# Optimization experiments

Measured on AMD Instinct MI355X. Metric: run time of the kernel, lower is better.

Reference implementation:

```python
import jax, jax.numpy as jnp
import numpy as np

N_EMBD = 1024
HEAD_SIZE = 64
BLOCK = 4096
B = 4

def setup_inputs() -> dict:
    key = jax.random.key(0)
    k1, k2, k3, k4, k5, k6 = jax.random.split(key, 6)
    x = jax.random.normal(k1, (B, BLOCK, N_EMBD), dtype=jnp.float32)
    freqs_cos = jax.random.uniform(k2, (BLOCK, HEAD_SIZE // 2), dtype=jnp.float32)
    freqs_sin = jax.random.uniform(k3, (BLOCK, HEAD_SIZE // 2), dtype=jnp.float32)
    # bias-free Linear weights, stored as [in, out] so y = x @ W
    s = 1.0 / np.sqrt(N_EMBD)
    Wq = jax.random.normal(k4, (N_EMBD, HEAD_SIZE), dtype=jnp.float32) * s
    Wk = jax.random.normal(k5, (N_EMBD, HEAD_SIZE), dtype=jnp.float32) * s
    Wv = jax.random.normal(k6, (N_EMBD, HEAD_SIZE), dtype=jnp.float32) * s
    return {"x": x, "Wq": Wq, "Wk": Wk, "Wv": Wv,
            "freqs_cos": freqs_cos, "freqs_sin": freqs_sin}

def _rope(t, cos, sin):
    # t: [B,T,hs]; cos/sin: [T, hs//2]. Rotate consecutive (even,odd) pairs.
    tr = t[..., 0::2]
    ti = t[..., 1::2]
    cos = cos[None, :, :]
    sin = sin[None, :, :]
    out_r = tr * cos - ti * sin
    out_i = tr * sin + ti * cos
    return jnp.stack([out_r, out_i], axis=-1).reshape(t.shape)

def reference(x, Wq, Wk, Wv, freqs_cos, freqs_sin):
    B_, T, C = x.shape
    q = x @ Wq  # [B,T,hs]
    k = x @ Wk
    v = x @ Wv
    q = _rope(q, freqs_cos[:T], freqs_sin[:T])
    k = _rope(k, freqs_cos[:T], freqs_sin[:T])
    scale = k.shape[-1] ** -0.5
    wei = jnp.einsum('bqd,bkd->bqk', q, k) * scale  # [B,T,T]
    mask = jnp.tril(jnp.ones((T, T), dtype=bool))
    wei = jnp.where(mask[None], wei, -jnp.inf)
    wei = jax.nn.softmax(wei, axis=-1)
    return jnp.einsum('bqk,bkd->bqd', wei, v)
```

## Files before the change

### kernel.cpp

```cpp
#include <hip/hip_runtime.h>
#include <hip/hip_bf16.h>
#include <stdint.h>

#define TSEQ 4096
#define CEMB 1024
#define DH   64
#define NB   4
#define NCHUNK 4

typedef __attribute__((ext_vector_type(8))) short bf16x8;
typedef __attribute__((ext_vector_type(4))) float f32x4;
typedef __attribute__((ext_vector_type(4))) float f4;
typedef unsigned short u16;

__device__ __forceinline__ u16 f2bf(float f) {
  __hip_bfloat16 h = __float2bfloat16(f);
  return *(u16*)&h;
}

__device__ __forceinline__ int swz(int row, int colbyte) {
  return row * 128 + (colbyte ^ ((row & 7) << 4));
}

__global__ void prep_w(const float* __restrict__ Wq, const float* __restrict__ Wk,
                       const float* __restrict__ Wv, u16* __restrict__ wt) {
  int idx = blockIdx.x * 256 + threadIdx.x;
  if (idx >= 3 * DH * CEMB) return;
  int m = idx >> 16;
  int r = idx & 65535;
  int k = r >> 6, n = r & 63;
  const float* W = (m == 0) ? Wq : (m == 1) ? Wk : Wv;
  wt[(size_t)m * 65536 + n * 1024 + k] = f2bf(W[r]);
}

__launch_bounds__(256)
__global__ void qkv_gemm(const float* __restrict__ x, const u16* __restrict__ wt,
                         const float* __restrict__ fc, const float* __restrict__ fs,
                         u16* __restrict__ q_ws, u16* __restrict__ k_ws,
                         u16* __restrict__ vt_ws) {
  const int tid  = threadIdx.x;
  const int lane = tid & 63;
  const int w    = tid >> 6;
  const int l15  = lane & 15;
  const int lhi  = lane >> 4;
  const int rg   = w & 1;
  const int cg   = w >> 1;
  const int m0   = blockIdx.x * 32;

  const float* xr = x + (size_t)(m0 + rg * 16 + l15) * CEMB;
  const u16*   wb = wt + (size_t)(cg * 96 + l15) * CEMB;

  const f32x4 z4 = {0.f, 0.f, 0.f, 0.f};
  f32x4 acc[6];
#pragma unroll
  for (int j = 0; j < 6; ++j) acc[j] = z4;

#pragma unroll 2
  for (int k0 = 0; k0 < CEMB; k0 += 64) {
    bf16x8 af[2];
#pragma unroll
    for (int kk = 0; kk < 2; ++kk) {
      const float* s = xr + k0 + kk * 32 + lhi * 8;
      f4 a = *(const f4*)s;
      f4 b = *(const f4*)(s + 4);
      af[kk][0] = (short)f2bf(a[0]); af[kk][1] = (short)f2bf(a[1]);
      af[kk][2] = (short)f2bf(a[2]); af[kk][3] = (short)f2bf(a[3]);
      af[kk][4] = (short)f2bf(b[0]); af[kk][5] = (short)f2bf(b[1]);
      af[kk][6] = (short)f2bf(b[2]); af[kk][7] = (short)f2bf(b[3]);
    }
#pragma unroll
    for (int kk = 0; kk < 2; ++kk)
#pragma unroll
      for (int nc = 0; nc < 6; ++nc) {
        bf16x8 bfr = *(const bf16x8*)(wb + (size_t)nc * 16 * CEMB + k0 + kk * 32 + lhi * 8);
        acc[nc] = __builtin_amdgcn_mfma_f32_16x16x32_bf16(af[kk], bfr, acc[nc], 0, 0, 0);
      }
  }

#pragma unroll
  for (int nc = 0; nc < 6; ++nc) {
    int gcol = cg * 96 + nc * 16 + l15;
    int mat  = gcol >> 6;
    int col  = gcol & 63;
#pragma unroll
    for (int r = 0; r < 4; ++r) {
      float v = acc[nc][r];
      float o = __shfl_xor(v, 1);
      int row = m0 + rg * 16 + lhi * 4 + r;
      int b = row >> 12, t = row & 4095;
      if (mat == 2) {
        vt_ws[((size_t)(b * DH + col)) * TSEQ + t] = f2bf(v);
      } else {
        int p = col >> 1;
        float cv = fc[t * 32 + p], sv = fs[t * 32 + p];
        float outv = ((col & 1) == 0) ? (v * cv - o * sv)
                                      : (o * sv + v * cv);
        if (mat == 0) outv *= 0.125f;
        u16* dst = (mat == 0) ? q_ws : k_ws;
        dst[(size_t)row * DH + col] = f2bf(outv);
      }
    }
  }
}

#define ATT_LOADKV(KV0) \
    _Pragma("unroll") for (int it = 0; it < 2; ++it) { \
      int gg = it * 256 + tid, row_ = gg >> 3, cc_ = gg & 7; \
      kreg[it] = *(const bf16x8*)(kb + (size_t)((KV0) + row_) * DH + cc_ * 8); \
      vreg[it] = *(const bf16x8*)(vb + (size_t)row_ * TSEQ + (KV0) + cc_ * 8); }
#define ATT_WRITEKV \
    _Pragma("unroll") for (int it = 0; it < 2; ++it) { \
      int gg = it * 256 + tid, row_ = gg >> 3, cc_ = gg & 7; \
      *(bf16x8*)((char*)kt + swz(row_, cc_ << 4)) = kreg[it]; \
      *(bf16x8*)((char*)vts + swz(row_, cc_ << 4)) = vreg[it]; }

__launch_bounds__(256)
__global__ void attn_partial(const u16* __restrict__ q_ws, const u16* __restrict__ k_ws,
                             const u16* __restrict__ vt_ws, float* __restrict__ po,
                             float* __restrict__ pml) {
  const int g  = blockIdx.x;
  const int j  = blockIdx.y;
  const int b  = g >> 6;
  const int r0 = g & 63;
  const int qt = (j & 1) ? (63 - r0) : r0;
  const int c  = j;

  const int ntiles = qt + 1;
  const int cnt    = (ntiles + NCHUNK - 1) / NCHUNK;
  const int t0     = c * cnt;
  if (t0 >= ntiles) return;
  const int t1     = min(t0 + cnt, ntiles);

  __shared__ __align__(16) u16 kt[64 * 64];
  __shared__ __align__(16) u16 vts[64 * 64];
  __shared__ __align__(16) u16 pt2[4 * 16 * 64];

  const int tid  = threadIdx.x;
  const int lane = tid & 63;
  const int w    = tid >> 6;
  const int l15  = lane & 15;
  const int lhi  = lane >> 4;
  const int q0   = qt * 64;

  const u16* qb = q_ws + (size_t)b * TSEQ * DH;
  const u16* kb = k_ws + (size_t)b * TSEQ * DH;
  const u16* vb = vt_ws + (size_t)b * DH * TSEQ;
  char* ptw = (char*)pt2 + w * 2048;

  bf16x8 aq[2];
  {
    int qrow = q0 + w * 16 + l15;
#pragma unroll
    for (int kk = 0; kk < 2; ++kk)
      aq[kk] = *(const bf16x8*)(qb + (size_t)qrow * DH + kk * 32 + lhi * 8);
  }

  const f32x4 z4 = {0.f, 0.f, 0.f, 0.f};
  f32x4 oacc[4] = {z4, z4, z4, z4};
  float m_r[4], l_p[4];
#pragma unroll
  for (int r = 0; r < 4; ++r) { m_r[r] = -1e30f; l_p[r] = 0.f; }

  const int myqbase = q0 + w * 16 + lhi * 4;

  bf16x8 kreg[2], vreg[2];

  for (int kv = t0; kv < t1; ++kv) {
    const int kv0 = kv * 64;
    ATT_LOADKV(kv0)
    __syncthreads();
    ATT_WRITEKV
    __syncthreads();

    f32x4 sacc[4] = {z4, z4, z4, z4};
    __builtin_amdgcn_s_setprio(1);
#pragma unroll
    for (int kk = 0; kk < 2; ++kk) {
#pragma unroll
      for (int cb = 0; cb < 4; ++cb) {
        bf16x8 bk = *(const bf16x8*)((char*)kt + swz(cb * 16 + l15, (kk * 32 + lhi * 8) * 2));
        sacc[cb] = __builtin_amdgcn_mfma_f32_16x16x32_bf16(aq[kk], bk, sacc[cb], 0, 0, 0);
      }
    }
    __builtin_amdgcn_s_setprio(0);

    if (kv0 == q0) {
#pragma unroll
      for (int cb = 0; cb < 4; ++cb)
#pragma unroll
        for (int r = 0; r < 4; ++r) {
          int ki = kv0 + cb * 16 + l15;
          int qi = myqbase + r;
          if (ki > qi) sacc[cb][r] = -1e30f;
        }
    }
    float mx[4];
#pragma unroll
    for (int r = 0; r < 4; ++r)
      mx[r] = fmaxf(fmaxf(sacc[0][r], sacc[1][r]), fmaxf(sacc[2][r], sacc[3][r]));
#pragma unroll
    for (int s = 1; s <= 8; s <<= 1)
#pragma unroll
      for (int r = 0; r < 4; ++r) mx[r] = fmaxf(mx[r], __shfl_xor(mx[r], s));
    bool skip = true;
#pragma unroll
    for (int r = 0; r < 4; ++r) skip = skip && (mx[r] <= m_r[r] + 8.f);
    if (!__all(skip)) {
#pragma unroll
      for (int r = 0; r < 4; ++r) {
        float mn = fmaxf(m_r[r], mx[r]);
        float fac = __expf(m_r[r] - mn);
        m_r[r] = mn;
        l_p[r] *= fac;
#pragma unroll
        for (int nc = 0; nc < 4; ++nc) oacc[nc][r] *= fac;
      }
    }
#pragma unroll
    for (int cb = 0; cb < 4; ++cb)
#pragma unroll
      for (int r = 0; r < 4; ++r) {
        float p = __expf(sacc[cb][r] - m_r[r]);
        l_p[r] += p;
        *(u16*)(ptw + swz(lhi * 4 + r, (cb * 16 + l15) * 2)) = f2bf(p);
      }
    bf16x8 ap[2];
#pragma unroll
    for (int kk = 0; kk < 2; ++kk)
      ap[kk] = *(const bf16x8*)(ptw + swz(l15, (kk * 32 + lhi * 8) * 2));
    __builtin_amdgcn_s_setprio(1);
#pragma unroll
    for (int kk = 0; kk < 2; ++kk)
#pragma unroll
      for (int nc = 0; nc < 4; ++nc) {
        bf16x8 bv = *(const bf16x8*)((char*)vts + swz(nc * 16 + l15, (kk * 32 + lhi * 8) * 2));
        oacc[nc] = __builtin_amdgcn_mfma_f32_16x16x32_bf16(ap[kk], bv, oacc[nc], 0, 0, 0);
      }
    __builtin_amdgcn_s_setprio(0);
  }

#pragma unroll
  for (int s = 1; s <= 8; s <<= 1)
#pragma unroll
    for (int r = 0; r < 4; ++r) l_p[r] += __shfl_xor(l_p[r], s);

  const int slot = ((b * 64 + qt) * NCHUNK + c);
  float* o_out = po + (size_t)slot * (64 * 64);
#pragma unroll
  for (int nc = 0; nc < 4; ++nc)
#pragma unroll
    for (int r = 0; r < 4; ++r) {
      int rloc = w * 16 + lhi * 4 + r;
      o_out[rloc * 64 + nc * 16 + l15] = oacc[nc][r];
    }
#pragma unroll
  for (int r = 0; r < 4; ++r) {
    if (l15 == 0) {
      int rloc = w * 16 + lhi * 4 + r;
      pml[(size_t)slot * 128 + rloc]      = m_r[r];
      pml[(size_t)slot * 128 + 64 + rloc] = l_p[r];
    }
  }
}

__launch_bounds__(256)
__global__ void attn_combine(const float* __restrict__ po, const float* __restrict__ pml,
                             float* __restrict__ out) {
  int idx = blockIdx.x * 256 + threadIdx.x;
  int d   = idx & 63;
  int t   = (idx >> 6) & 4095;
  int b   = idx >> 18;
  int qt  = t >> 6;
  int rloc = t & 63;
  int ntiles = qt + 1;
  int cnt = (ntiles + NCHUNK - 1) / NCHUNK;

  float m_c[NCHUNK], l_c[NCHUNK], o_c[NCHUNK];
  float M = -1e30f;
#pragma unroll
  for (int c = 0; c < NCHUNK; ++c) {
    bool valid = (c * cnt < ntiles);
    int slot = ((b * 64 + qt) * NCHUNK + c);
    m_c[c] = valid ? pml[(size_t)slot * 128 + rloc]      : -1e30f;
    l_c[c] = valid ? pml[(size_t)slot * 128 + 64 + rloc] : 0.f;
    o_c[c] = valid ? po[(size_t)slot * (64 * 64) + rloc * 64 + d] : 0.f;
    M = fmaxf(M, m_c[c]);
  }
  float den = 0.f, num = 0.f;
#pragma unroll
  for (int c = 0; c < NCHUNK; ++c) {
    float e = __expf(m_c[c] - M);
    den += e * l_c[c];
    num += e * o_c[c];
  }
  out[idx] = num / den;
}

extern "C" void kernel_launch(void* const* d_in, const int* in_sizes, int n_in,
                              void* d_out, int out_size, void* d_ws, size_t ws_size,
                              hipStream_t stream) {
  const float* x  = (const float*)d_in[0];
  const float* Wq = (const float*)d_in[1];
  const float* Wk = (const float*)d_in[2];
  const float* Wv = (const float*)d_in[3];
  const float* fc = (const float*)d_in[4];
  const float* fs = (const float*)d_in[5];
  float* out = (float*)d_out;

  char* ws = (char*)d_ws;
  u16*   wt    = (u16*)(ws);
  u16*   q_ws  = (u16*)(ws + (1u << 19));
  u16*   k_ws  = (u16*)(ws + (1u << 19) + (1u << 21));
  u16*   vt_ws = (u16*)(ws + (1u << 19) + (2u << 21));
  float* po    = (float*)(ws + (1u << 19) + (3u << 21));
  float* pml   = (float*)(ws + (1u << 19) + (3u << 21) + (1u << 24));

  prep_w<<<(3 * DH * CEMB + 255) / 256, 256, 0, stream>>>(Wq, Wk, Wv, wt);
  qkv_gemm<<<dim3(512), 256, 0, stream>>>(x, wt, fc, fs, q_ws, k_ws, vt_ws);
  attn_partial<<<dim3(256, NCHUNK), 256, 0, stream>>>(q_ws, k_ws, vt_ws, po, pml);
  attn_combine<<<dim3((NB * TSEQ * DH) / 256), 256, 0, stream>>>(po, pml, out);
}
```

Baseline: 192.7 us.

## Pre-swizzle weights into MFMA fragment order and double-buffer QKV GEMM loads

The weight prep kernel now writes bf16 weights already arranged in per-lane MFMA B-fragment order, so each lane reads a contiguous 16-byte chunk and a wave's load is fully coalesced. The QKV GEMM main loop is rewritten as a software-pipelined, double-buffered loop that issues the next k-step's x and weight loads before running the current step's MFMAs, to hide global-load latency. Launch bounds now request two blocks per CU. The two register buffers raise register pressure, which could limit occupancy or cause spills.

```diff
diff --git a/kernel.cpp b/kernel.cpp
--- a/kernel.cpp
+++ b/kernel.cpp
@@ -23,18 +23,36 @@
 }
 
 __global__ void prep_w(const float* __restrict__ Wq, const float* __restrict__ Wk,
-                       const float* __restrict__ Wv, u16* __restrict__ wt) {
+                       const float* __restrict__ Wv, u16* __restrict__ wf) {
   int idx = blockIdx.x * 256 + threadIdx.x;
   if (idx >= 3 * DH * CEMB) return;
-  int m = idx >> 16;
-  int r = idx & 65535;
-  int k = r >> 6, n = r & 63;
-  const float* W = (m == 0) ? Wq : (m == 1) ? Wk : Wv;
-  wt[(size_t)m * 65536 + n * 1024 + k] = f2bf(W[r]);
-}
-
-__launch_bounds__(256)
-__global__ void qkv_gemm(const float* __restrict__ x, const u16* __restrict__ wt,
+  int j    = idx & 7;
+  int lane = (idx >> 3) & 63;
+  int ku   = (idx >> 9) & 31;
+  int ncg  = idx >> 14;
+  int col_g = ncg * 16 + (lane & 15);
+  int k     = ku * 32 + (lane >> 4) * 8 + j;
+  int mat = col_g >> 6, n = col_g & 63;
+  const float* W = (mat == 0) ? Wq : (mat == 1) ? Wk : Wv;
+  wf[idx] = f2bf(W[k * DH + n]);
+}
+
+#define LOADB(DST, U) \
+    _Pragma("unroll") for (int nc = 0; nc < 6; ++nc) \
+      DST[nc] = *(const bf16x8*)(wfb + (((size_t)nc * 32 + (size_t)(U)) << 9));
+#define LOADA(FA, FB, U) { const float* s_ = xr + (U) * 32; \
+    FA = *(const f4*)s_; FB = *(const f4*)(s_ + 4); }
+#define CVT_MFMA(FA, FB, B) { \
+    bf16x8 af_; \
+    af_[0] = (short)f2bf(FA[0]); af_[1] = (short)f2bf(FA[1]); \
+    af_[2] = (short)f2bf(FA[2]); af_[3] = (short)f2bf(FA[3]); \
+    af_[4] = (short)f2bf(FB[0]); af_[5] = (short)f2bf(FB[1]); \
+    af_[6] = (short)f2bf(FB[2]); af_[7] = (short)f2bf(FB[3]); \
+    _Pragma("unroll") for (int nc = 0; nc < 6; ++nc) \
+      acc[nc] = __builtin_amdgcn_mfma_f32_16x16x32_bf16(af_, B[nc], acc[nc], 0, 0, 0); }
+
+__launch_bounds__(256, 2)
+__global__ void qkv_gemm(const float* __restrict__ x, const u16* __restrict__ wf,
                          const float* __restrict__ fc, const float* __restrict__ fs,
                          u16* __restrict__ q_ws, u16* __restrict__ k_ws,
                          u16* __restrict__ vt_ws) {
@@ -47,34 +65,25 @@
   const int cg   = w >> 1;
   const int m0   = blockIdx.x * 32;
 
-  const float* xr = x + (size_t)(m0 + rg * 16 + l15) * CEMB;
-  const u16*   wb = wt + (size_t)(cg * 96 + l15) * CEMB;
+  const float* xr  = x + (size_t)(m0 + rg * 16 + l15) * CEMB + lhi * 8;
+  const u16*   wfb = wf + (((size_t)(cg * 6) * 32) << 9) + lane * 8;
 
   const f32x4 z4 = {0.f, 0.f, 0.f, 0.f};
   f32x4 acc[6];
 #pragma unroll
   for (int j = 0; j < 6; ++j) acc[j] = z4;
 
-#pragma unroll 2
-  for (int k0 = 0; k0 < CEMB; k0 += 64) {
-    bf16x8 af[2];
-#pragma unroll
-    for (int kk = 0; kk < 2; ++kk) {
-      const float* s = xr + k0 + kk * 32 + lhi * 8;
-      f4 a = *(const f4*)s;
-      f4 b = *(const f4*)(s + 4);
-      af[kk][0] = (short)f2bf(a[0]); af[kk][1] = (short)f2bf(a[1]);
-      af[kk][2] = (short)f2bf(a[2]); af[kk][3] = (short)f2bf(a[3]);
-      af[kk][4] = (short)f2bf(b[0]); af[kk][5] = (short)f2bf(b[1]);
-      af[kk][6] = (short)f2bf(b[2]); af[kk][7] = (short)f2bf(b[3]);
-    }
-#pragma unroll
-    for (int kk = 0; kk < 2; ++kk)
-#pragma unroll
-      for (int nc = 0; nc < 6; ++nc) {
-        bf16x8 bfr = *(const bf16x8*)(wb + (size_t)nc * 16 * CEMB + k0 + kk * 32 + lhi * 8);
-        acc[nc] = __builtin_amdgcn_mfma_f32_16x16x32_bf16(af[kk], bfr, acc[nc], 0, 0, 0);
-      }
+  bf16x8 Ba[6], Bb[6];
+  f4 a0, a1, b0, b1;
+
+  LOADB(Ba, 0) LOADA(a0, a1, 0)
+  LOADB(Bb, 1) LOADA(b0, b1, 1)
+
+  for (int u = 0; u < 32; u += 2) {
+    CVT_MFMA(a0, a1, Ba)
+    if (u + 2 < 32) { LOADB(Ba, u + 2) LOADA(a0, a1, u + 2) }
+    CVT_MFMA(b0, b1, Bb)
+    if (u + 3 < 32) { LOADB(Bb, u + 3) LOADA(b0, b1, u + 3) }
   }
 
 #pragma unroll
@@ -308,15 +317,15 @@
   float* out = (float*)d_out;
 
   char* ws = (char*)d_ws;
-  u16*   wt    = (u16*)(ws);
+  u16*   wf    = (u16*)(ws);
   u16*   q_ws  = (u16*)(ws + (1u << 19));
   u16*   k_ws  = (u16*)(ws + (1u << 19) + (1u << 21));
   u16*   vt_ws = (u16*)(ws + (1u << 19) + (2u << 21));
   float* po    = (float*)(ws + (1u << 19) + (3u << 21));
   float* pml   = (float*)(ws + (1u << 19) + (3u << 21) + (1u << 24));
 
-  prep_w<<<(3 * DH * CEMB + 255) / 256, 256, 0, stream>>>(Wq, Wk, Wv, wt);
-  qkv_gemm<<<dim3(512), 256, 0, stream>>>(x, wt, fc, fs, q_ws, k_ws, vt_ws);
+  prep_w<<<(3 * DH * CEMB + 255) / 256, 256, 0, stream>>>(Wq, Wk, Wv, wf);
+  qkv_gemm<<<dim3(512), 256, 0, stream>>>(x, wf, fc, fs, q_ws, k_ws, vt_ws);
   attn_partial<<<dim3(256, NCHUNK), 256, 0, stream>>>(q_ws, k_ws, vt_ws, po, pml);
   attn_combine<<<dim3((NB * TSEQ * DH) / 256), 256, 0, stream>>>(po, pml, out);
 }
```

Result: faster. 172.0 us (-10.7%).
